# Kernel tuning notes

Hardware: AMD Instinct MI355X
Metric: run time of the kernel (lower is better)

## Reference

```python
import jax, jax.numpy as jnp
import numpy as np

X_SIZE = 256
H_SIZE = 512
N_CHILDREN = 32768


def setup_inputs() -> dict:
    key = jax.random.key(0)
    ks = jax.random.split(key, 7)
    x = jax.random.normal(ks[0], (X_SIZE,), dtype=jnp.float32)
    hs = jax.random.normal(ks[1], (N_CHILDREN, H_SIZE), dtype=jnp.float32)
    cs = jax.random.normal(ks[2], (N_CHILDREN, H_SIZE), dtype=jnp.float32)
    # xavier-uniform-ish init for weights, zeros for biases
    def xavier(k, shape):
        fan_in, fan_out = shape[-1], shape[-2]
        limit = float(np.sqrt(6.0 / (fan_in + fan_out)))
        return jax.random.uniform(k, shape, jnp.float32, -limit, limit)
    w_iou = xavier(ks[3], (3, H_SIZE, X_SIZE))
    u_iou = xavier(ks[4], (3, H_SIZE, H_SIZE))
    b_iou = jnp.zeros((3, H_SIZE), jnp.float32)
    w_f = xavier(ks[5], (H_SIZE, X_SIZE))
    u_f = xavier(ks[6], (H_SIZE, H_SIZE))
    b_f = jnp.zeros((H_SIZE, 1), jnp.float32)
    return {"x": x, "hs": hs, "cs": cs, "w_iou": w_iou, "u_iou": u_iou,
            "b_iou": b_iou, "w_f": w_f, "u_f": u_f, "b_f": b_f}


def reference(x, hs, cs, w_iou, u_iou, b_iou, w_f, u_f, b_f):
    # Child-sum Tree-LSTM cell for a single node.
    h_sum = hs.sum(axis=0)                                    # (h,)
    iou = (jnp.einsum('khx,x->kh', w_iou, x)
           + jnp.einsum('khg,g->kh', u_iou, h_sum)
           + b_iou)                                            # (3, h)
    i, o, u = iou[0], iou[1], iou[2]
    # fs: (h, n_children) forget gates, one per child
    fs = (w_f @ x)[:, None] + jnp.einsum('hg,ng->hn', u_f, hs) + b_f
    i = jax.nn.sigmoid(i)
    o = jax.nn.sigmoid(o)
    fs = jax.nn.sigmoid(fs)
    u = jnp.tanh(u)
    c = i * u + jnp.sum(fs * cs.T, axis=1)                    # (h,)
    h = o * jnp.tanh(c)
    return (h, c)
```

## Files before the change

### kernel.cpp

```cpp
#include <hip/hip_runtime.h>
#include <stdint.h>
#include <stddef.h>

#define H 512
#define XD 256
#define NCHLD 32768
#define NB 64
#define KT 32
#define NKT 16
#define NCT 4
#define NRT 4
#define LDSP 40
#define NSHARD 4

#define WS_PREF 0
#define WS_CACC 512
#define WS_HSUM 2560
#define WS_IOU  4608
#define WS_UF16 8192

typedef float f32x4 __attribute__((ext_vector_type(4)));
typedef _Float16 f16x8 __attribute__((ext_vector_type(8)));
typedef _Float16 f16x4 __attribute__((ext_vector_type(4)));

__device__ __forceinline__ float sigm(float x) { return 1.0f / (1.0f + __expf(-x)); }

__global__ __launch_bounds__(256) void k0_setup(const float* __restrict__ x,
                                                const float* __restrict__ w_f,
                                                const float* __restrict__ b_f,
                                                const float* __restrict__ u_f,
                                                float* __restrict__ ws) {
    const int b = blockIdx.x;
    if (b < 256) {
        const int i = (b * 256 + threadIdx.x) * 4;
        float4 v = *(const float4*)(u_f + i);
        f16x4 h;
        h[0] = (_Float16)v.x; h[1] = (_Float16)v.y;
        h[2] = (_Float16)v.z; h[3] = (_Float16)v.w;
        *(f16x4*)((_Float16*)(ws + WS_UF16) + i) = h;
    } else {
        const int gid = (b - 256) * 256 + threadIdx.x;
        const int row = gid >> 2;
        const int part = gid & 3;
        const float4* wr = (const float4*)(w_f + (size_t)row * XD) + part * 16;
        const float4* xv = (const float4*)x + part * 16;
        float acc = 0.0f;
#pragma unroll 4
        for (int i = 0; i < 16; ++i) {
            float4 a = wr[i], c = xv[i];
            acc += a.x * c.x + a.y * c.y + a.z * c.z + a.w * c.w;
        }
        acc += __shfl_xor(acc, 1);
        acc += __shfl_xor(acc, 2);
        if (part == 0) ws[WS_PREF + row] = acc + b_f[row];
        ws[WS_CACC + gid] = 0.0f;
        ws[WS_HSUM + gid] = 0.0f;
    }
}

__global__ __launch_bounds__(512, 4) void k2_main(const float* __restrict__ hs,
                                                  const float* __restrict__ cs,
                                                  float* __restrict__ ws) {
    __shared__ _Float16 bt[2][NB][LDSP];
    __shared__ float hsum_l[H];

    const _Float16* uf16 = (const _Float16*)(ws + WS_UF16);
    const float* pre_f = ws + WS_PREF;
    float* c_acc = ws + WS_CACC + (blockIdx.x & (NSHARD - 1)) * H;
    float* h_sum = ws + WS_HSUM + (blockIdx.x & (NSHARD - 1)) * H;

    const int tid  = threadIdx.x;
    const int wid  = tid >> 6;
    const int lane = tid & 63;
    const int c0   = blockIdx.x * NB;

    const int sc  = tid >> 3;
    const int skg = tid & 7;
    const float* hsrc = hs + (size_t)(c0 + sc) * H + skg * 4;
    _Float16* stp0 = &bt[0][sc][skg * 4];
    _Float16* stp1 = &bt[1][sc][skg * 4];

    const int arow = wid * 64 + (lane & 15);
    const int ak   = (lane >> 4) * 8;
    const _Float16* abase = uf16 + (size_t)arow * H + ak;

    const int bcol = lane & 15;
    const int bk   = (lane >> 4) * 8;

    f32x4 acc[NRT][NCT];
    const f32x4 vzero = {0.0f, 0.0f, 0.0f, 0.0f};
#pragma unroll
    for (int rt = 0; rt < NRT; ++rt)
#pragma unroll
        for (int ct = 0; ct < NCT; ++ct)
            acc[rt][ct] = vzero;

    if (tid < H) hsum_l[tid] = 0.0f;

    float4 ra = *(const float4*)(hsrc);
    float4 rb = *(const float4*)(hsrc + KT);
    __syncthreads();

    {
        f16x4 h;
        h[0] = (_Float16)ra.x; h[1] = (_Float16)ra.y;
        h[2] = (_Float16)ra.z; h[3] = (_Float16)ra.w;
        *(f16x4*)stp0 = h;
        float4 v = ra;
#pragma unroll
        for (int m = 8; m <= 32; m <<= 1) {
            v.x += __shfl_xor(v.x, m); v.y += __shfl_xor(v.y, m);
            v.z += __shfl_xor(v.z, m); v.w += __shfl_xor(v.w, m);
        }
        if ((lane >> 3) == 0) {
            const int d = skg * 4;
            atomicAdd(&hsum_l[d + 0], v.x); atomicAdd(&hsum_l[d + 1], v.y);
            atomicAdd(&hsum_l[d + 2], v.z); atomicAdd(&hsum_l[d + 3], v.w);
        }
    }
    __syncthreads();

#pragma unroll
    for (int kk = 0; kk < NKT; ++kk) {
        if (kk + 2 < NKT) ra = *(const float4*)(hsrc + (size_t)(kk + 2) * KT);

        f16x8 af[NRT];
#pragma unroll
        for (int rt = 0; rt < NRT; ++rt)
            af[rt] = *(const f16x8*)(abase + (size_t)rt * 16 * H + kk * KT);

        const _Float16* bbase = &bt[kk & 1][0][0];
#pragma unroll
        for (int ct = 0; ct < NCT; ++ct) {
            f16x8 bf = *(const f16x8*)(bbase + (ct * 16 + bcol) * LDSP + bk);
#pragma unroll
            for (int rt = 0; rt < NRT; ++rt)
                acc[rt][ct] = __builtin_amdgcn_mfma_f32_16x16x32_f16(af[rt], bf, acc[rt][ct], 0, 0, 0);
        }

        if (kk + 1 < NKT) {
            _Float16* stp = (kk & 1) ? stp0 : stp1;
            f16x4 h;
            h[0] = (_Float16)rb.x; h[1] = (_Float16)rb.y;
            h[2] = (_Float16)rb.z; h[3] = (_Float16)rb.w;
            *(f16x4*)stp = h;
            float4 v = rb;
#pragma unroll
            for (int m = 8; m <= 32; m <<= 1) {
                v.x += __shfl_xor(v.x, m); v.y += __shfl_xor(v.y, m);
                v.z += __shfl_xor(v.z, m); v.w += __shfl_xor(v.w, m);
            }
            if ((lane >> 3) == 0) {
                const int d = (kk + 1) * KT + skg * 4;
                atomicAdd(&hsum_l[d + 0], v.x); atomicAdd(&hsum_l[d + 1], v.y);
                atomicAdd(&hsum_l[d + 2], v.z); atomicAdd(&hsum_l[d + 3], v.w);
            }
        }
        __syncthreads();
        rb = ra;
    }

    if (tid < H) atomicAdd(&h_sum[tid], hsum_l[tid]);

    const int g4 = (lane >> 4) * 4;
#pragma unroll
    for (int rt = 0; rt < NRT; ++rt) {
        const int rbase = wid * 64 + rt * 16 + g4;
        float4 pf = *(const float4*)(pre_f + rbase);
        f32x4 csum = vzero;
#pragma unroll
        for (int ct = 0; ct < NCT; ++ct) {
            const int child = c0 + ct * 16 + (lane & 15);
            float4 cv = *(const float4*)(cs + (size_t)child * H + rbase);
            csum[0] += sigm(acc[rt][ct][0] + pf.x) * cv.x;
            csum[1] += sigm(acc[rt][ct][1] + pf.y) * cv.y;
            csum[2] += sigm(acc[rt][ct][2] + pf.z) * cv.z;
            csum[3] += sigm(acc[rt][ct][3] + pf.w) * cv.w;
        }
#pragma unroll
        for (int m = 1; m <= 8; m <<= 1) {
            csum[0] += __shfl_xor(csum[0], m); csum[1] += __shfl_xor(csum[1], m);
            csum[2] += __shfl_xor(csum[2], m); csum[3] += __shfl_xor(csum[3], m);
        }
        if ((lane & 15) == 0) {
            atomicAdd(&c_acc[rbase + 0], csum[0]); atomicAdd(&c_acc[rbase + 1], csum[1]);
            atomicAdd(&c_acc[rbase + 2], csum[2]); atomicAdd(&c_acc[rbase + 3], csum[3]);
        }
    }
}

__global__ __launch_bounds__(256) void k3_iou(const float* __restrict__ x,
                                              const float* __restrict__ w_iou,
                                              const float* __restrict__ u_iou,
                                              const float* __restrict__ b_iou,
                                              float* __restrict__ ws) {
    const int gid = blockIdx.x * 256 + threadIdx.x;
    const int row = gid >> 3;
    const int part = gid & 7;
    float acc = 0.0f;
    const float4* wr = (const float4*)(w_iou + (size_t)row * XD) + part * 8;
    const float4* xv = (const float4*)x + part * 8;
#pragma unroll
    for (int i = 0; i < 8; ++i) {
        float4 a = wr[i], b = xv[i];
        acc += a.x * b.x + a.y * b.y + a.z * b.z + a.w * b.w;
    }
    const float4* ur = (const float4*)(u_iou + (size_t)row * H) + part * 16;
    const float4* h0 = (const float4*)(ws + WS_HSUM) + part * 16;
    const float4* h1 = h0 + 128;
    const float4* h2 = h1 + 128;
    const float4* h3 = h2 + 128;
#pragma unroll 4
    for (int i = 0; i < 16; ++i) {
        float4 a = ur[i];
        float4 b0 = h0[i], b1 = h1[i], b2 = h2[i], b3 = h3[i];
        acc += a.x * (b0.x + b1.x + b2.x + b3.x);
        acc += a.y * (b0.y + b1.y + b2.y + b3.y);
        acc += a.z * (b0.z + b1.z + b2.z + b3.z);
        acc += a.w * (b0.w + b1.w + b2.w + b3.w);
    }
    acc += __shfl_xor(acc, 1);
    acc += __shfl_xor(acc, 2);
    acc += __shfl_xor(acc, 4);
    if (part == 0) ws[WS_IOU + row] = acc + b_iou[row];
}

__global__ __launch_bounds__(512) void k4_fin(const float* __restrict__ ws,
                                              float* __restrict__ out) {
    const int h = threadIdx.x;
    const float i = sigm(ws[WS_IOU + h]);
    const float o = sigm(ws[WS_IOU + 512 + h]);
    const float u = tanhf(ws[WS_IOU + 1024 + h]);
    const float cacc = ws[WS_CACC + h] + ws[WS_CACC + 512 + h] +
                       ws[WS_CACC + 1024 + h] + ws[WS_CACC + 1536 + h];
    const float c = i * u + cacc;
    out[h]       = o * tanhf(c);
    out[512 + h] = c;
}

extern "C" void kernel_launch(void* const* d_in, const int* in_sizes, int n_in,
                              void* d_out, int out_size, void* d_ws, size_t ws_size,
                              hipStream_t stream) {
    const float* x     = (const float*)d_in[0];
    const float* hs    = (const float*)d_in[1];
    const float* cs    = (const float*)d_in[2];
    const float* w_iou = (const float*)d_in[3];
    const float* u_iou = (const float*)d_in[4];
    const float* b_iou = (const float*)d_in[5];
    const float* w_f   = (const float*)d_in[6];
    const float* u_f   = (const float*)d_in[7];
    const float* b_f   = (const float*)d_in[8];
    float* ws  = (float*)d_ws;
    float* out = (float*)d_out;

    k0_setup<<<264, 256, 0, stream>>>(x, w_f, b_f, u_f, ws);
    k2_main<<<NCHLD / NB, 512, 0, stream>>>(hs, cs, ws);
    k3_iou<<<48, 256, 0, stream>>>(x, w_iou, u_iou, b_iou, ws);
    k4_fin<<<1, 512, 0, stream>>>(ws, out);
}
```

Baseline: 213.6 us.

## Stage full hs tile into LDS upfront, drop per-k-step barriers

The main kernel now loads each block's whole 64x512 slice of hs into LDS as fp16 in one prologue, with 8 float4 loads kept in flight per thread. This replaces the double-buffered 32-wide k-slices that needed a barrier on every step, so the MFMA loop runs without synchronization. The cost is much larger LDS use (about 66KB per block), which may lower occupancy, and the global-load/MFMA overlap inside a block is lost. The iou kernel is also split across twice as many threads per row, and the zero-init in setup now uses float4 stores.

```diff
diff --git a/kernel.cpp b/kernel.cpp
--- a/kernel.cpp
+++ b/kernel.cpp
@@ -6,11 +6,9 @@
 #define XD 256
 #define NCHLD 32768
 #define NB 64
-#define KT 32
-#define NKT 16
 #define NCT 4
 #define NRT 4
-#define LDSP 40
+#define LDSP 520
 #define NSHARD 4
 
 #define WS_PREF 0
@@ -53,15 +51,17 @@
         acc += __shfl_xor(acc, 1);
         acc += __shfl_xor(acc, 2);
         if (part == 0) ws[WS_PREF + row] = acc + b_f[row];
-        ws[WS_CACC + gid] = 0.0f;
-        ws[WS_HSUM + gid] = 0.0f;
+        if (gid < 512) {
+            ((float4*)(ws + WS_CACC))[gid] = make_float4(0.f, 0.f, 0.f, 0.f);
+            ((float4*)(ws + WS_HSUM))[gid] = make_float4(0.f, 0.f, 0.f, 0.f);
+        }
     }
 }
 
 __global__ __launch_bounds__(512, 4) void k2_main(const float* __restrict__ hs,
                                                   const float* __restrict__ cs,
                                                   float* __restrict__ ws) {
-    __shared__ _Float16 bt[2][NB][LDSP];
+    __shared__ _Float16 bt[NB][LDSP];
     __shared__ float hsum_l[H];
 
     const _Float16* uf16 = (const _Float16*)(ws + WS_UF16);
@@ -74,93 +74,82 @@
     const int lane = tid & 63;
     const int c0   = blockIdx.x * NB;
 
-    const int sc  = tid >> 3;
-    const int skg = tid & 7;
-    const float* hsrc = hs + (size_t)(c0 + sc) * H + skg * 4;
-    _Float16* stp0 = &bt[0][sc][skg * 4];
-    _Float16* stp1 = &bt[1][sc][skg * 4];
+    const int sc = tid >> 3;
+    const int sg = tid & 7;
+    const float* hsrc = hs + (size_t)(c0 + sc) * H + sg * 4;
+    _Float16* stp = &bt[sc][sg * 4];
+
+    if (tid < H) hsum_l[tid] = 0.0f;
+    __syncthreads();
+
+    float4 r[8];
+#pragma unroll
+    for (int s = 0; s < 8; ++s) r[s] = *(const float4*)(hsrc + (size_t)s * 32);
+
+#define STAGE_SLICE(vv, s)                                                        \
+    {                                                                             \
+        f16x4 hq;                                                                 \
+        hq[0] = (_Float16)(vv).x; hq[1] = (_Float16)(vv).y;                       \
+        hq[2] = (_Float16)(vv).z; hq[3] = (_Float16)(vv).w;                       \
+        *(f16x4*)(stp + (s) * 32) = hq;                                           \
+        float4 v = (vv);                                                          \
+        v.x += __shfl_xor(v.x, 8);  v.y += __shfl_xor(v.y, 8);                    \
+        v.z += __shfl_xor(v.z, 8);  v.w += __shfl_xor(v.w, 8);                    \
+        v.x += __shfl_xor(v.x, 16); v.y += __shfl_xor(v.y, 16);                   \
+        v.z += __shfl_xor(v.z, 16); v.w += __shfl_xor(v.w, 16);                   \
+        v.x += __shfl_xor(v.x, 32); v.y += __shfl_xor(v.y, 32);                   \
+        v.z += __shfl_xor(v.z, 32); v.w += __shfl_xor(v.w, 32);                   \
+        if (lane < 8) {                                                           \
+            const int d = (s) * 32 + sg * 4;                                      \
+            atomicAdd(&hsum_l[d + 0], v.x); atomicAdd(&hsum_l[d + 1], v.y);       \
+            atomicAdd(&hsum_l[d + 2], v.z); atomicAdd(&hsum_l[d + 3], v.w);       \
+        }                                                                         \
+    }
+
+#pragma unroll
+    for (int s = 0; s < 8; ++s) {
+        float4 vv = r[s];
+        r[s] = *(const float4*)(hsrc + (size_t)(s + 8) * 32);
+        STAGE_SLICE(vv, s)
+    }
+#pragma unroll
+    for (int s = 0; s < 8; ++s) {
+        STAGE_SLICE(r[s], s + 8)
+    }
+#undef STAGE_SLICE
+
+    __syncthreads();
+
+    atomicAdd(&h_sum[tid], hsum_l[tid]);
+
+    f32x4 acc[NRT][NCT];
+    const f32x4 vzero = {0.0f, 0.0f, 0.0f, 0.0f};
+#pragma unroll
+    for (int rt = 0; rt < NRT; ++rt)
+#pragma unroll
+        for (int ct = 0; ct < NCT; ++ct)
+            acc[rt][ct] = vzero;
 
     const int arow = wid * 64 + (lane & 15);
     const int ak   = (lane >> 4) * 8;
     const _Float16* abase = uf16 + (size_t)arow * H + ak;
-
     const int bcol = lane & 15;
     const int bk   = (lane >> 4) * 8;
 
-    f32x4 acc[NRT][NCT];
-    const f32x4 vzero = {0.0f, 0.0f, 0.0f, 0.0f};
-#pragma unroll
-    for (int rt = 0; rt < NRT; ++rt)
-#pragma unroll
-        for (int ct = 0; ct < NCT; ++ct)
-            acc[rt][ct] = vzero;
-
-    if (tid < H) hsum_l[tid] = 0.0f;
-
-    float4 ra = *(const float4*)(hsrc);
-    float4 rb = *(const float4*)(hsrc + KT);
-    __syncthreads();
-
-    {
-        f16x4 h;
-        h[0] = (_Float16)ra.x; h[1] = (_Float16)ra.y;
-        h[2] = (_Float16)ra.z; h[3] = (_Float16)ra.w;
-        *(f16x4*)stp0 = h;
-        float4 v = ra;
-#pragma unroll
-        for (int m = 8; m <= 32; m <<= 1) {
-            v.x += __shfl_xor(v.x, m); v.y += __shfl_xor(v.y, m);
-            v.z += __shfl_xor(v.z, m); v.w += __shfl_xor(v.w, m);
-        }
-        if ((lane >> 3) == 0) {
-            const int d = skg * 4;
-            atomicAdd(&hsum_l[d + 0], v.x); atomicAdd(&hsum_l[d + 1], v.y);
-            atomicAdd(&hsum_l[d + 2], v.z); atomicAdd(&hsum_l[d + 3], v.w);
-        }
-    }
-    __syncthreads();
-
-#pragma unroll
-    for (int kk = 0; kk < NKT; ++kk) {
-        if (kk + 2 < NKT) ra = *(const float4*)(hsrc + (size_t)(kk + 2) * KT);
-
+#pragma unroll
+    for (int kk = 0; kk < 16; ++kk) {
         f16x8 af[NRT];
 #pragma unroll
         for (int rt = 0; rt < NRT; ++rt)
-            af[rt] = *(const f16x8*)(abase + (size_t)rt * 16 * H + kk * KT);
-
-        const _Float16* bbase = &bt[kk & 1][0][0];
+            af[rt] = *(const f16x8*)(abase + (size_t)rt * 16 * H + kk * 32);
 #pragma unroll
         for (int ct = 0; ct < NCT; ++ct) {
-            f16x8 bf = *(const f16x8*)(bbase + (ct * 16 + bcol) * LDSP + bk);
+            f16x8 bf = *(const f16x8*)(&bt[ct * 16 + bcol][kk * 32 + bk]);
 #pragma unroll
             for (int rt = 0; rt < NRT; ++rt)
                 acc[rt][ct] = __builtin_amdgcn_mfma_f32_16x16x32_f16(af[rt], bf, acc[rt][ct], 0, 0, 0);
         }
-
-        if (kk + 1 < NKT) {
-            _Float16* stp = (kk & 1) ? stp0 : stp1;
-            f16x4 h;
-            h[0] = (_Float16)rb.x; h[1] = (_Float16)rb.y;
-            h[2] = (_Float16)rb.z; h[3] = (_Float16)rb.w;
-            *(f16x4*)stp = h;
-            float4 v = rb;
-#pragma unroll
-            for (int m = 8; m <= 32; m <<= 1) {
-                v.x += __shfl_xor(v.x, m); v.y += __shfl_xor(v.y, m);
-                v.z += __shfl_xor(v.z, m); v.w += __shfl_xor(v.w, m);
-            }
-            if ((lane >> 3) == 0) {
-                const int d = (kk + 1) * KT + skg * 4;
-                atomicAdd(&hsum_l[d + 0], v.x); atomicAdd(&hsum_l[d + 1], v.y);
-                atomicAdd(&hsum_l[d + 2], v.z); atomicAdd(&hsum_l[d + 3], v.w);
-            }
-        }
-        __syncthreads();
-        rb = ra;
-    }
-
-    if (tid < H) atomicAdd(&h_sum[tid], hsum_l[tid]);
+    }
 
     const int g4 = (lane >> 4) * 4;
 #pragma unroll
@@ -195,23 +184,23 @@
                                               const float* __restrict__ b_iou,
                                               float* __restrict__ ws) {
     const int gid = blockIdx.x * 256 + threadIdx.x;
-    const int row = gid >> 3;
-    const int part = gid & 7;
+    const int row = gid >> 4;
+    const int part = gid & 15;
     float acc = 0.0f;
-    const float4* wr = (const float4*)(w_iou + (size_t)row * XD) + part * 8;
-    const float4* xv = (const float4*)x + part * 8;
-#pragma unroll
-    for (int i = 0; i < 8; ++i) {
+    const float4* wr = (const float4*)(w_iou + (size_t)row * XD) + part * 4;
+    const float4* xv = (const float4*)x + part * 4;
+#pragma unroll
+    for (int i = 0; i < 4; ++i) {
         float4 a = wr[i], b = xv[i];
         acc += a.x * b.x + a.y * b.y + a.z * b.z + a.w * b.w;
     }
-    const float4* ur = (const float4*)(u_iou + (size_t)row * H) + part * 16;
-    const float4* h0 = (const float4*)(ws + WS_HSUM) + part * 16;
+    const float4* ur = (const float4*)(u_iou + (size_t)row * H) + part * 8;
+    const float4* h0 = (const float4*)(ws + WS_HSUM) + part * 8;
     const float4* h1 = h0 + 128;
     const float4* h2 = h1 + 128;
     const float4* h3 = h2 + 128;
-#pragma unroll 4
-    for (int i = 0; i < 16; ++i) {
+#pragma unroll
+    for (int i = 0; i < 8; ++i) {
         float4 a = ur[i];
         float4 b0 = h0[i], b1 = h1[i], b2 = h2[i], b3 = h3[i];
         acc += a.x * (b0.x + b1.x + b2.x + b3.x);
@@ -222,6 +211,7 @@
     acc += __shfl_xor(acc, 1);
     acc += __shfl_xor(acc, 2);
     acc += __shfl_xor(acc, 4);
+    acc += __shfl_xor(acc, 8);
     if (part == 0) ws[WS_IOU + row] = acc + b_iou[row];
 }
 
@@ -255,6 +245,6 @@
 
     k0_setup<<<264, 256, 0, stream>>>(x, w_f, b_f, u_f, ws);
     k2_main<<<NCHLD / NB, 512, 0, stream>>>(hs, cs, ws);
-    k3_iou<<<48, 256, 0, stream>>>(x, w_iou, u_iou, b_iou, ws);
+    k3_iou<<<96, 256, 0, stream>>>(x, w_iou, u_iou, b_iou, ws);
     k4_fin<<<1, 512, 0, stream>>>(ws, out);
 }
```

Measured after the change: 209.3 us. 1.02x faster.
